# Performance work log

Measured on AMD Instinct MI355X. Metric: run time of the kernel, lower is better.

The kernel has to match this reference:

```python
import jax, jax.numpy as jnp
import numpy as np

UNITS = 512
GROUPS = 32
EPS = 1e-5


def group_norm(x, w, b, groups=GROUPS, eps=EPS):
    B, C, H, W = x.shape
    xg = x.reshape(B, groups, C // groups, H, W)
    mean = xg.mean(axis=(2, 3, 4), keepdims=True)
    var = ((xg - mean) ** 2).mean(axis=(2, 3, 4), keepdims=True)
    xg = (xg - mean) * jax.lax.rsqrt(var + eps)
    return xg.reshape(B, C, H, W) * w[None, :, None, None] + b[None, :, None, None]


def conv1x1(x, w, b):
    # w: [out_ch, in_ch], b: [out_ch]
    return jnp.einsum('oc,bchw->bohw', w, x) + b[None, :, None, None]


def setup_inputs() -> dict:
    key = jax.random.key(0)
    ks = jax.random.split(key, 11)
    C = UNITS
    s = 1.0 / np.sqrt(C)
    return {
        'x': jax.random.normal(ks[0], (16, C, 64, 64), dtype=jnp.float32),
        'gn_w': jnp.ones((C,), dtype=jnp.float32),
        'gn_b': jnp.zeros((C,), dtype=jnp.float32),
        'wq': jax.random.normal(ks[1], (C, C), dtype=jnp.float32) * s,
        'bq': jnp.zeros((C,), dtype=jnp.float32),
        'wk': jax.random.normal(ks[2], (C, C), dtype=jnp.float32) * s,
        'bk': jnp.zeros((C,), dtype=jnp.float32),
        'wv': jax.random.normal(ks[3], (C, C), dtype=jnp.float32) * s,
        'bv': jnp.zeros((C,), dtype=jnp.float32),
        'wp': jax.random.normal(ks[4], (C, C), dtype=jnp.float32) * s,
        'bp': jnp.zeros((C,), dtype=jnp.float32),
    }


def reference(x, gn_w, gn_b, wq, bq, wk, bk, wv, bv, wp, bp):
    B, C, H, W = x.shape
    g = GROUPS
    xn = group_norm(x, gn_w, gn_b)
    q = conv1x1(xn, wq, bq).reshape(B, g, C // g, H * W)
    k = conv1x1(xn, wk, bk).reshape(B, g, C // g, H * W)
    v = conv1x1(xn, wv, bv).reshape(B, g, C // g, H * W)
    # channel attention: scores over per-group channel dims, spatial contracted
    attn = jnp.einsum('bgci,bgdi->bgcd', q, k) / jnp.sqrt(jnp.float32(C))
    attn = jax.nn.softmax(attn, axis=-1)
    out = jnp.einsum('bgcd,bgdi->bgci', attn, v).reshape(B, C, H, W)
    # NB: original adds proj(out) to out (not a residual to the input)
    return out + conv1x1(out, wp, bp)
```

## Files before the change

### kernel.cpp

```cpp
#include <hip/hip_runtime.h>

typedef __attribute__((ext_vector_type(8))) short bf16x8;
typedef __attribute__((ext_vector_type(4))) float f32x4;
typedef __attribute__((ext_vector_type(8))) unsigned short us8;
typedef unsigned short u16;
typedef unsigned int u32;

__device__ __forceinline__ u16 f2bf(float f){
  u32 u = __builtin_bit_cast(u32, f);
  u32 r = (u + 0x7fffu + ((u >> 16) & 1u)) >> 16;
  return (u16)r;
}

#define ASYNC_CP16(gp, lp) __builtin_amdgcn_global_load_lds( \
    (__attribute__((address_space(1))) void*)(gp), \
    (__attribute__((address_space(3))) void*)(lp), 16, 0, 0)

__device__ const int d_rt[10] = {0,0,0,0,1,1,1,2,2,3};
__device__ const int d_ct[10] = {0,1,2,3,1,2,3,2,3,3};

__global__ __launch_bounds__(256) void k_stats(const float* __restrict__ x,
    const float* __restrict__ gnw, const float* __restrict__ gnb,
    u16* __restrict__ xb, float* __restrict__ a, float* __restrict__ cv,
    float* __restrict__ sx)
{
  int b = blockIdx.x >> 5;
  int g = blockIdx.x & 31;
  int tid = threadIdx.x;
  int cl = tid >> 4;
  int l16 = tid & 15;
  int c = g * 16 + cl;
  const float* xp = x + ((long)(b * 512 + c)) * 4096;
  u16* xbp = xb + ((long)(b * 512 + c)) * 4096;
  float s = 0.f, sq = 0.f;
  for (int it = 0; it < 64; ++it) {
    int i4 = it * 16 + l16;
    float4 v = *(const float4*)(xp + i4 * 4);
    s  += v.x + v.y + v.z + v.w;
    sq += v.x * v.x + v.y * v.y + v.z * v.z + v.w * v.w;
    ushort4 o;
    o.x = f2bf(v.x); o.y = f2bf(v.y); o.z = f2bf(v.z); o.w = f2bf(v.w);
    *(ushort4*)(xbp + i4 * 4) = o;
  }
  for (int off = 8; off; off >>= 1) { s += __shfl_xor(s, off); sq += __shfl_xor(sq, off); }
  __shared__ float chS[16], chQ[16];
  if (l16 == 0) { chS[cl] = s; chQ[cl] = sq; }
  __syncthreads();
  if (tid < 16) {
    float S = 0.f, Q = 0.f;
    for (int j = 0; j < 16; ++j) { S += chS[j]; Q += chQ[j]; }
    float mean = S * (1.f / 65536.f);
    float var  = Q * (1.f / 65536.f) - mean * mean;
    float rs = rsqrtf(var + 1e-5f);
    int cc = g * 16 + tid;
    float av = gnw[cc] * rs;
    a[b * 512 + cc]  = av;
    cv[b * 512 + cc] = gnb[cc] - mean * av;
    sx[b * 512 + cc] = chS[tid];
  }
}

__global__ __launch_bounds__(256) void k_wconv(const float* __restrict__ wq,
    const float* __restrict__ wp, u16* __restrict__ wqb, u16* __restrict__ wpb)
{
  int i = blockIdx.x * 256 + threadIdx.x;
  wqb[i] = f2bf(wq[i]);
  wpb[i] = f2bf(wp[i]);
}

__global__ __launch_bounds__(256) void k_transpose(const u16* __restrict__ xb,
                                                   u16* __restrict__ xT)
{
  __shared__ u16 t[64][72];
  int i0 = blockIdx.x * 64, e0 = blockIdx.y * 64, b = blockIdx.z;
  int tid = threadIdx.x;
  #pragma unroll
  for (int p = 0; p < 2; ++p) {
    int task = p * 256 + tid;
    int er = task >> 3, ic = (task & 7) * 8;
    us8 v = *(const us8*)(xb + ((long)(b * 512 + e0 + er)) * 4096 + i0 + ic);
    #pragma unroll
    for (int j = 0; j < 8; ++j) t[ic + j][er] = v[j];
  }
  __syncthreads();
  #pragma unroll
  for (int p = 0; p < 2; ++p) {
    int task = p * 256 + tid;
    int ir = task >> 3, ec = (task & 7) * 8;
    us8 w = *(const us8*)&t[ir][ec];
    *(us8*)(xT + ((long)(b * 4096 + i0 + ir)) * 512 + e0 + ec) = w;
  }
}

__global__ __launch_bounds__(256) void k_gram_split(const u16* __restrict__ xb,
                                                    float* __restrict__ part)
{
  __shared__ u16 As[128 * 64];
  __shared__ u16 Bs[128 * 64];
  const int tid = threadIdx.x;
  const int wave = tid >> 6, lane = tid & 63;
  const int tile = blockIdx.x % 10, split = blockIdx.x / 10;
  const int b = blockIdx.y;
  const int tm = d_rt[tile] * 128, tn = d_ct[tile] * 128;
  const u16* Xb = xb + (long)b * 512 * 4096;
  const int wm = (wave >> 1) << 6, wn = (wave & 1) << 6;
  const int l15 = lane & 15, l4 = lane >> 4;

  f32x4 acc[4][4];
  f32x4 z = {0.f, 0.f, 0.f, 0.f};
  #pragma unroll
  for (int fm = 0; fm < 4; ++fm)
    #pragma unroll
    for (int fn = 0; fn < 4; ++fn) acc[fm][fn] = z;

  const int qa = wave * 4;
  const int srow = lane >> 3;
  const int scol = (lane & 7) * 8;
  const int k0 = split * 1024;

  for (int kt = k0; kt < k0 + 1024; kt += 64) {
    #pragma unroll
    for (int j = 0; j < 4; ++j) {
      int q = qa + j;
      const u16* gpA = Xb + (long)(tm + q * 8 + srow) * 4096 + kt + scol;
      ASYNC_CP16(gpA, &As[q * 512]);
      const u16* gpB = Xb + (long)(tn + q * 8 + srow) * 4096 + kt + scol;
      ASYNC_CP16(gpB, &Bs[q * 512]);
    }
    __syncthreads();
    #pragma unroll
    for (int kk = 0; kk < 64; kk += 32) {
      bf16x8 af[4], bfr[4];
      #pragma unroll
      for (int f = 0; f < 4; ++f) {
        af[f]  = *(const bf16x8*)&As[(wm + f * 16 + l15) * 64 + kk + l4 * 8];
        bfr[f] = *(const bf16x8*)&Bs[(wn + f * 16 + l15) * 64 + kk + l4 * 8];
      }
      #pragma unroll
      for (int fm = 0; fm < 4; ++fm)
        #pragma unroll
        for (int fn = 0; fn < 4; ++fn)
          acc[fm][fn] = __builtin_amdgcn_mfma_f32_16x16x32_bf16(
              af[fm], bfr[fn], acc[fm][fn], 0, 0, 0);
    }
    __syncthreads();
  }

  float* pp = part + ((((long)split * 16 + b) * 10 + tile) << 14);
  #pragma unroll
  for (int fm = 0; fm < 4; ++fm)
    #pragma unroll
    for (int fn = 0; fn < 4; ++fn)
      #pragma unroll
      for (int r = 0; r < 4; ++r)
        pp[(wm + fm * 16 + l4 * 4 + r) * 128 + wn + fn * 16 + l15] =
            acc[fm][fn][r];
}

__global__ __launch_bounds__(512) void k_gram_reduce(
    const float* __restrict__ part, const float* __restrict__ a,
    u16* __restrict__ Gp)
{
  const int tile = blockIdx.x, b = blockIdx.y;
  const int tmt = d_rt[tile], tnt = d_ct[tile];
  const int tm = tmt * 128, tn = tnt * 128;
  const int tid = threadIdx.x;
  __shared__ u16 t[128][130];
  const float* p0 = part + (((long)b * 10 + tile) << 14);
  const long ss = (long)16 * 10 * 16384;
  u16* Gb = Gp + (long)b * 262144;
  const float acol = a[b * 512 + tn + (tid & 127)];
  for (int chunk = 0; chunk < 32; ++chunk) {
    int idx = chunk * 512 + tid;
    int row = idx >> 7, col = idx & 127;
    float v = p0[idx] + p0[idx + ss] + p0[idx + 2 * ss] + p0[idx + 3 * ss];
    v *= a[b * 512 + tm + row] * acol;
    u16 bf = f2bf(v);
    Gb[(tm + row) * 512 + tn + col] = bf;
    t[row][col] = bf;
  }
  if (tmt != tnt) {
    __syncthreads();
    for (int chunk = 0; chunk < 32; ++chunk) {
      int idx = chunk * 512 + tid;
      int row = idx >> 7, col = idx & 127;
      Gb[(tn + row) * 512 + tm + col] = t[col][row];
    }
  }
}

template<int EPI>
__global__ __launch_bounds__(256) void k_ntgemm(
    const u16* __restrict__ A, long sA, int lda,
    const u16* __restrict__ B, long sB, int ldb,
    int K, int ntn,
    float* __restrict__ fout, long sF, int ldf,
    u16* __restrict__ bout, long sO, int ldo_,
    const float* __restrict__ ascale,
    const float* __restrict__ cinit,
    const float* __restrict__ cadd)
{
  __shared__ u16 As[128 * 64];
  __shared__ u16 Bs[128 * 64];
  const int tid = threadIdx.x;
  const int wave = tid >> 6, lane = tid & 63;
  const int b = blockIdx.y;
  const int tm = (blockIdx.x / ntn) * 128, tn = (blockIdx.x % ntn) * 128;
  const u16* Ab = A + sA * b;
  const u16* Bb = B + sB * b;
  const int wm = (wave >> 1) << 6, wn = (wave & 1) << 6;
  const int l15 = lane & 15, l4 = lane >> 4;

  f32x4 acc[4][4];
  if (EPI == 2) {
    const float* Cb = cinit + (long)b * 262144;
    #pragma unroll
    for (int fm = 0; fm < 4; ++fm)
      #pragma unroll
      for (int fn = 0; fn < 4; ++fn)
        #pragma unroll
        for (int r = 0; r < 4; ++r) {
          int row = tm + wm + fm * 16 + l4 * 4 + r;
          int col = tn + wn + fn * 16 + l15;
          acc[fm][fn][r] = Cb[row * 512 + col];
        }
  } else {
    f32x4 z = {0.f, 0.f, 0.f, 0.f};
    #pragma unroll
    for (int fm = 0; fm < 4; ++fm)
      #pragma unroll
      for (int fn = 0; fn < 4; ++fn) acc[fm][fn] = z;
  }

  const int qa = wave * 4;
  const int srow = lane >> 3;
  const int scol = (lane & 7) * 8;

  for (int kt = 0; kt < K; kt += 64) {
    #pragma unroll
    for (int j = 0; j < 4; ++j) {
      int q = qa + j;
      const u16* gpA = Ab + (long)(tm + q * 8 + srow) * lda + kt + scol;
      ASYNC_CP16(gpA, &As[q * 512]);
      const u16* gpB = Bb + (long)(tn + q * 8 + srow) * ldb + kt + scol;
      ASYNC_CP16(gpB, &Bs[q * 512]);
    }
    __syncthreads();
    #pragma unroll
    for (int kk = 0; kk < 64; kk += 32) {
      bf16x8 af[4], bfr[4];
      #pragma unroll
      for (int f = 0; f < 4; ++f) {
        af[f]  = *(const bf16x8*)&As[(wm + f * 16 + l15) * 64 + kk + l4 * 8];
        bfr[f] = *(const bf16x8*)&Bs[(wn + f * 16 + l15) * 64 + kk + l4 * 8];
      }
      #pragma unroll
      for (int fm = 0; fm < 4; ++fm)
        #pragma unroll
        for (int fn = 0; fn < 4; ++fn)
          acc[fm][fn] = __builtin_amdgcn_mfma_f32_16x16x32_bf16(
              af[fm], bfr[fn], acc[fm][fn], 0, 0, 0);
    }
    __syncthreads();
  }

  #pragma unroll
  for (int fm = 0; fm < 4; ++fm)
    #pragma unroll
    for (int fn = 0; fn < 4; ++fn)
      #pragma unroll
      for (int r = 0; r < 4; ++r) {
        int row = tm + wm + fm * 16 + l4 * 4 + r;
        int col = tn + wn + fn * 16 + l15;
        float v = acc[fm][fn][r];
        if (EPI == 1) {
          fout[sF * b + (long)row * ldf + col] = v;
        } else if (EPI == 2) {
          v *= ascale[b * 512 + col];
          bout[sO * b + (long)row * ldo_ + col] = f2bf(v);
        } else {
          fout[sF * b + (long)row * ldf + col] = v + cadd[b * 512 + row];
        }
      }
}

__global__ __launch_bounds__(256) void k_vec(
    const float* __restrict__ wq, const float* __restrict__ bq,
    const float* __restrict__ wk, const float* __restrict__ bk,
    const float* __restrict__ wv, const float* __restrict__ bv,
    const float* __restrict__ a, const float* __restrict__ cv,
    const float* __restrict__ sx,
    float* __restrict__ eq, float* __restrict__ uq, float* __restrict__ ek,
    float* __restrict__ uk, float* __restrict__ hv)
{
  int b = blockIdx.x / 5, which = blockIdx.x % 5;
  __shared__ float vec[512];
  int tid = threadIdx.x;
  for (int i = tid; i < 512; i += 256)
    vec[i] = (which == 1 || which == 3) ? a[b * 512 + i] * sx[b * 512 + i]
                                        : cv[b * 512 + i];
  __syncthreads();
  const float* W = (which < 2) ? wq : (which < 4) ? wk : wv;
  const float* bias = (which == 0) ? bq : (which == 2) ? bk : (which == 4) ? bv : nullptr;
  float* outp = (which == 0) ? eq : (which == 1) ? uq : (which == 2) ? ek
              : (which == 3) ? uk : hv;
  for (int c = tid; c < 512; c += 256) {
    const float* wr = W + (long)c * 512;
    float s2 = 0.f;
    for (int e = 0; e < 512; e += 4) {
      float4 w4 = *(const float4*)(wr + e);
      s2 += w4.x * vec[e] + w4.y * vec[e + 1] + w4.z * vec[e + 2] + w4.w * vec[e + 3];
    }
    if (bias) s2 += bias[c];
    outp[b * 512 + c] = s2;
  }
}

__global__ __launch_bounds__(256) void k_scores(
    const float* __restrict__ P,
    const float* __restrict__ wk, const float* __restrict__ wv,
    const float* __restrict__ eq, const float* __restrict__ uq,
    const float* __restrict__ ek, const float* __restrict__ uk,
    const float* __restrict__ hv,
    float* __restrict__ U, u16* __restrict__ UT, float* __restrict__ oc)
{
  int b = blockIdx.x >> 5, g = blockIdx.x & 31;
  int tid = threadIdx.x;
  __shared__ float Pl[16 * 516];
  __shared__ float Wl[16 * 516];
  __shared__ float at[16][16];

  const float* Pb = P + (long)b * 262144 + g * 16 * 512;
  for (int t = tid; t < 16 * 128; t += 256) {
    int r = t >> 7, q = t & 127;
    *(float4*)&Pl[r * 516 + q * 4] = *(const float4*)(Pb + r * 512 + q * 4);
  }
  const float* Wkb = wk + (long)g * 16 * 512;
  for (int t = tid; t < 16 * 128; t += 256) {
    int r = t >> 7, q = t & 127;
    *(float4*)&Wl[r * 516 + q * 4] = *(const float4*)(Wkb + r * 512 + q * 4);
  }
  __syncthreads();

  int c = tid >> 4, d = tid & 15;
  float s0 = 0.f;
  for (int e = 0; e < 512; e += 4) {
    float4 p4 = *(const float4*)&Pl[c * 516 + e];
    float4 w4 = *(const float4*)&Wl[d * 516 + e];
    s0 += p4.x * w4.x + p4.y * w4.y + p4.z * w4.z + p4.w * w4.w;
  }
  float eqc = eq[b * 512 + g * 16 + c], uqc = uq[b * 512 + g * 16 + c];
  float ekd = ek[b * 512 + g * 16 + d], ukd = uk[b * 512 + g * 16 + d];
  float s = (s0 + eqc * ukd + uqc * ekd + 4096.f * eqc * ekd) * 0.04419417382415922f;
  float m = s;
  for (int off = 8; off; off >>= 1) m = fmaxf(m, __shfl_xor(m, off));
  float p = expf(s - m);
  float sum = p;
  for (int off = 8; off; off >>= 1) sum += __shfl_xor(sum, off);
  at[c][d] = p / sum;
  __syncthreads();

  const float* Wvb = wv + (long)g * 16 * 512;
  for (int t = tid; t < 16 * 128; t += 256) {
    int r = t >> 7, q = t & 127;
    *(float4*)&Wl[r * 516 + q * 4] = *(const float4*)(Wvb + r * 512 + q * 4);
  }
  __syncthreads();

  float* Ub = U + (long)b * 262144 + g * 16 * 512;
  for (int t = 0; t < 32; ++t) {
    int flat = t * 256 + tid;
    int cc = flat >> 9, e = flat & 511;
    float a2 = 0.f;
    #pragma unroll
    for (int dd = 0; dd < 16; ++dd) a2 += at[cc][dd] * Wl[dd * 516 + e];
    Ub[cc * 512 + e] = a2;
    Pl[cc * 516 + e] = a2;
  }
  if (tid < 16) {
    float o2 = 0.f;
    #pragma unroll
    for (int dd = 0; dd < 16; ++dd) o2 += at[tid][dd] * hv[b * 512 + g * 16 + dd];
    oc[b * 512 + g * 16 + tid] = o2;
  }
  __syncthreads();
  for (int t = 0; t < 32; ++t) {
    int flat = t * 256 + tid;
    int cc = flat & 15, e = flat >> 4;
    UT[(long)b * 262144 + e * 512 + g * 16 + cc] = f2bf(Pl[cc * 516 + e]);
  }
}

__global__ __launch_bounds__(256) void k_c3(const float* __restrict__ wp,
    const float* __restrict__ bp, const float* __restrict__ oc,
    float* __restrict__ c3)
{
  int b = blockIdx.x >> 1;
  int o = (blockIdx.x & 1) * 256 + threadIdx.x;
  __shared__ float ov[512];
  for (int i = threadIdx.x; i < 512; i += 256) ov[i] = oc[b * 512 + i];
  __syncthreads();
  const float* wr = wp + (long)o * 512;
  float s = 0.f;
  for (int e = 0; e < 512; e += 4) {
    float4 w4 = *(const float4*)(wr + e);
    s += w4.x * ov[e] + w4.y * ov[e + 1] + w4.z * ov[e + 2] + w4.w * ov[e + 3];
  }
  c3[b * 512 + o] = oc[b * 512 + o] + s + bp[o];
}

extern "C" void kernel_launch(void* const* d_in, const int* in_sizes, int n_in,
                              void* d_out, int out_size, void* d_ws, size_t ws_size,
                              hipStream_t stream)
{
  (void)in_sizes; (void)n_in; (void)out_size; (void)ws_size;
  const float* x   = (const float*)d_in[0];
  const float* gnw = (const float*)d_in[1];
  const float* gnb = (const float*)d_in[2];
  const float* wq  = (const float*)d_in[3];
  const float* bq  = (const float*)d_in[4];
  const float* wk  = (const float*)d_in[5];
  const float* bk  = (const float*)d_in[6];
  const float* wv  = (const float*)d_in[7];
  const float* bv  = (const float*)d_in[8];
  const float* wp  = (const float*)d_in[9];
  const float* bp  = (const float*)d_in[10];
  float* out = (float*)d_out;

  char* ws = (char*)d_ws;
  u16* xT  = (u16*)ws;  ws += (size_t)16 * 4096 * 512 * 2;
  u16* Gp  = (u16*)ws;  ws += (size_t)16 * 512 * 512 * 2;
  float* P = (float*)ws; ws += (size_t)16 * 512 * 512 * 4;
  float* U = (float*)ws; ws += (size_t)16 * 512 * 512 * 4;
  u16* UT  = (u16*)ws;  ws += (size_t)16 * 512 * 512 * 2;
  u16* W3  = (u16*)ws;  ws += (size_t)16 * 512 * 512 * 2;
  u16* wqb = (u16*)ws;  ws += (size_t)512 * 512 * 2;
  u16* wpb = (u16*)ws;  ws += (size_t)512 * 512 * 2;
  float* a  = (float*)ws; ws += 16 * 512 * 4;
  float* cv = (float*)ws; ws += 16 * 512 * 4;
  float* sx = (float*)ws; ws += 16 * 512 * 4;
  float* eq = (float*)ws; ws += 16 * 512 * 4;
  float* uq = (float*)ws; ws += 16 * 512 * 4;
  float* ek = (float*)ws; ws += 16 * 512 * 4;
  float* uk = (float*)ws; ws += 16 * 512 * 4;
  float* hv = (float*)ws; ws += 16 * 512 * 4;
  float* oc = (float*)ws; ws += 16 * 512 * 4;
  float* c3 = (float*)ws; ws += 16 * 512 * 4;

  u16* xb = (u16*)d_out;
  float* part = (float*)xT;

  k_stats<<<512, 256, 0, stream>>>(x, gnw, gnb, xb, a, cv, sx);
  k_wconv<<<1024, 256, 0, stream>>>(wq, wp, wqb, wpb);
  k_gram_split<<<dim3(40, 16), 256, 0, stream>>>(xb, part);
  k_gram_reduce<<<dim3(10, 16), 512, 0, stream>>>(part, a, Gp);
  k_transpose<<<dim3(64, 8, 16), 256, 0, stream>>>(xb, xT);
  k_vec<<<80, 256, 0, stream>>>(wq, bq, wk, bk, wv, bv, a, cv, sx,
                                eq, uq, ek, uk, hv);
  k_ntgemm<1><<<dim3(16, 16), 256, 0, stream>>>(
      wqb, 0, 512, Gp, 262144, 512, 512, 4,
      P, 262144, 512, nullptr, 0, 0, nullptr, nullptr, nullptr);
  k_scores<<<512, 256, 0, stream>>>(P, wk, wv, eq, uq, ek, uk, hv, U, UT, oc);
  k_c3<<<32, 256, 0, stream>>>(wp, bp, oc, c3);
  k_ntgemm<2><<<dim3(16, 16), 256, 0, stream>>>(
      wpb, 0, 512, UT, 262144, 512, 512, 4,
      nullptr, 0, 0, W3, 262144, 512, a, U, nullptr);
  k_ntgemm<3><<<dim3(128, 16), 256, 0, stream>>>(
      W3, 262144, 512, xT, (long)4096 * 512, 512, 512, 32,
      out, (long)512 * 4096, 4096, nullptr, 0, 0, nullptr, nullptr, c3);
}
```

Baseline: 299.6 us.

## Double-buffer LDS in GEMM kernels, share diagonal gram tiles, store P as bf16

Both the gram-split and generic NT GEMM kernels now use two LDS buffers, so the next K-tile's async global-to-LDS copy is issued while the current tile feeds the MFMAs. Diagonal gram tiles load only the A tile and reuse it as B, which halves their global traffic. The intermediate P matrix is written as bf16 instead of fp32 and widened back to fp32 in k_scores, cutting its memory traffic at some cost in precision. Doubling LDS use (64KB per block) may lower occupancy. The loop issues the next stage's async writes without waiting on them before reading the current buffer, which depends on the implicit vmcnt handling of global_load_lds.

```diff
diff --git a/kernel.cpp b/kernel.cpp
--- a/kernel.cpp
+++ b/kernel.cpp
@@ -10,6 +10,9 @@
   u32 u = __builtin_bit_cast(u32, f);
   u32 r = (u + 0x7fffu + ((u >> 16) & 1u)) >> 16;
   return (u16)r;
+}
+__device__ __forceinline__ float bf2f(u16 h){
+  return __builtin_bit_cast(float, (u32)h << 16);
 }
 
 #define ASYNC_CP16(gp, lp) __builtin_amdgcn_global_load_lds( \
@@ -95,12 +98,13 @@
 __global__ __launch_bounds__(256) void k_gram_split(const u16* __restrict__ xb,
                                                     float* __restrict__ part)
 {
-  __shared__ u16 As[128 * 64];
-  __shared__ u16 Bs[128 * 64];
+  __shared__ u16 As[2][128 * 64];
+  __shared__ u16 Bs[2][128 * 64];
   const int tid = threadIdx.x;
   const int wave = tid >> 6, lane = tid & 63;
   const int tile = blockIdx.x % 10, split = blockIdx.x / 10;
   const int b = blockIdx.y;
+  const bool diag = (d_rt[tile] == d_ct[tile]);
   const int tm = d_rt[tile] * 128, tn = d_ct[tile] * 128;
   const u16* Xb = xb + (long)b * 512 * 4096;
   const int wm = (wave >> 1) << 6, wn = (wave & 1) << 6;
@@ -116,25 +120,34 @@
   const int qa = wave * 4;
   const int srow = lane >> 3;
   const int scol = (lane & 7) * 8;
-  const int k0 = split * 1024;
-
-  for (int kt = k0; kt < k0 + 1024; kt += 64) {
+  const int k0 = split * 1024, kend = k0 + 1024;
+
+  auto STAGE = [&](int buf, int kt) {
     #pragma unroll
     for (int j = 0; j < 4; ++j) {
       int q = qa + j;
-      const u16* gpA = Xb + (long)(tm + q * 8 + srow) * 4096 + kt + scol;
-      ASYNC_CP16(gpA, &As[q * 512]);
-      const u16* gpB = Xb + (long)(tn + q * 8 + srow) * 4096 + kt + scol;
-      ASYNC_CP16(gpB, &Bs[q * 512]);
-    }
-    __syncthreads();
+      ASYNC_CP16(Xb + (long)(tm + q * 8 + srow) * 4096 + kt + scol,
+                 &As[buf][q * 512]);
+      if (!diag)
+        ASYNC_CP16(Xb + (long)(tn + q * 8 + srow) * 4096 + kt + scol,
+                   &Bs[buf][q * 512]);
+    }
+  };
+
+  STAGE(0, k0);
+  __syncthreads();
+  int cur = 0;
+  for (int kt = k0; kt < kend; kt += 64) {
+    if (kt + 64 < kend) STAGE(cur ^ 1, kt + 64);
+    const u16* cA = &As[cur][0];
+    const u16* cB = diag ? cA : &Bs[cur][0];
     #pragma unroll
     for (int kk = 0; kk < 64; kk += 32) {
       bf16x8 af[4], bfr[4];
       #pragma unroll
       for (int f = 0; f < 4; ++f) {
-        af[f]  = *(const bf16x8*)&As[(wm + f * 16 + l15) * 64 + kk + l4 * 8];
-        bfr[f] = *(const bf16x8*)&Bs[(wn + f * 16 + l15) * 64 + kk + l4 * 8];
+        af[f]  = *(const bf16x8*)&cA[(wm + f * 16 + l15) * 64 + kk + l4 * 8];
+        bfr[f] = *(const bf16x8*)&cB[(wn + f * 16 + l15) * 64 + kk + l4 * 8];
       }
       #pragma unroll
       for (int fm = 0; fm < 4; ++fm)
@@ -144,6 +157,7 @@
               af[fm], bfr[fn], acc[fm][fn], 0, 0, 0);
     }
     __syncthreads();
+    cur ^= 1;
   }
 
   float* pp = part + ((((long)split * 16 + b) * 10 + tile) << 14);
@@ -200,8 +214,8 @@
     const float* __restrict__ cinit,
     const float* __restrict__ cadd)
 {
-  __shared__ u16 As[128 * 64];
-  __shared__ u16 Bs[128 * 64];
+  __shared__ u16 As[2][128 * 64];
+  __shared__ u16 Bs[2][128 * 64];
   const int tid = threadIdx.x;
   const int wave = tid >> 6, lane = tid & 63;
   const int b = blockIdx.y;
@@ -236,23 +250,29 @@
   const int srow = lane >> 3;
   const int scol = (lane & 7) * 8;
 
-  for (int kt = 0; kt < K; kt += 64) {
+  auto STAGE = [&](int buf, int kt) {
     #pragma unroll
     for (int j = 0; j < 4; ++j) {
       int q = qa + j;
-      const u16* gpA = Ab + (long)(tm + q * 8 + srow) * lda + kt + scol;
-      ASYNC_CP16(gpA, &As[q * 512]);
-      const u16* gpB = Bb + (long)(tn + q * 8 + srow) * ldb + kt + scol;
-      ASYNC_CP16(gpB, &Bs[q * 512]);
-    }
-    __syncthreads();
+      ASYNC_CP16(Ab + (long)(tm + q * 8 + srow) * lda + kt + scol,
+                 &As[buf][q * 512]);
+      ASYNC_CP16(Bb + (long)(tn + q * 8 + srow) * ldb + kt + scol,
+                 &Bs[buf][q * 512]);
+    }
+  };
+
+  STAGE(0, 0);
+  __syncthreads();
+  int cur = 0;
+  for (int kt = 0; kt < K; kt += 64) {
+    if (kt + 64 < K) STAGE(cur ^ 1, kt + 64);
     #pragma unroll
     for (int kk = 0; kk < 64; kk += 32) {
       bf16x8 af[4], bfr[4];
       #pragma unroll
       for (int f = 0; f < 4; ++f) {
-        af[f]  = *(const bf16x8*)&As[(wm + f * 16 + l15) * 64 + kk + l4 * 8];
-        bfr[f] = *(const bf16x8*)&Bs[(wn + f * 16 + l15) * 64 + kk + l4 * 8];
+        af[f]  = *(const bf16x8*)&As[cur][(wm + f * 16 + l15) * 64 + kk + l4 * 8];
+        bfr[f] = *(const bf16x8*)&Bs[cur][(wn + f * 16 + l15) * 64 + kk + l4 * 8];
       }
       #pragma unroll
       for (int fm = 0; fm < 4; ++fm)
@@ -262,6 +282,7 @@
               af[fm], bfr[fn], acc[fm][fn], 0, 0, 0);
     }
     __syncthreads();
+    cur ^= 1;
   }
 
   #pragma unroll
@@ -274,7 +295,7 @@
         int col = tn + wn + fn * 16 + l15;
         float v = acc[fm][fn][r];
         if (EPI == 1) {
-          fout[sF * b + (long)row * ldf + col] = v;
+          bout[sO * b + (long)row * ldo_ + col] = f2bf(v);
         } else if (EPI == 2) {
           v *= ascale[b * 512 + col];
           bout[sO * b + (long)row * ldo_ + col] = f2bf(v);
@@ -317,7 +338,7 @@
 }
 
 __global__ __launch_bounds__(256) void k_scores(
-    const float* __restrict__ P,
+    const u16* __restrict__ P,
     const float* __restrict__ wk, const float* __restrict__ wv,
     const float* __restrict__ eq, const float* __restrict__ uq,
     const float* __restrict__ ek, const float* __restrict__ uk,
@@ -330,10 +351,12 @@
   __shared__ float Wl[16 * 516];
   __shared__ float at[16][16];
 
-  const float* Pb = P + (long)b * 262144 + g * 16 * 512;
-  for (int t = tid; t < 16 * 128; t += 256) {
-    int r = t >> 7, q = t & 127;
-    *(float4*)&Pl[r * 516 + q * 4] = *(const float4*)(Pb + r * 512 + q * 4);
+  const u16* Pb = P + (long)b * 262144 + g * 16 * 512;
+  for (int t = tid; t < 1024; t += 256) {
+    int r = t >> 6, q = (t & 63) * 8;
+    us8 v = *(const us8*)(Pb + r * 512 + q);
+    #pragma unroll
+    for (int j = 0; j < 8; ++j) Pl[r * 516 + q + j] = bf2f(v[j]);
   }
   const float* Wkb = wk + (long)g * 16 * 512;
   for (int t = tid; t < 16 * 128; t += 256) {
@@ -430,7 +453,7 @@
   char* ws = (char*)d_ws;
   u16* xT  = (u16*)ws;  ws += (size_t)16 * 4096 * 512 * 2;
   u16* Gp  = (u16*)ws;  ws += (size_t)16 * 512 * 512 * 2;
-  float* P = (float*)ws; ws += (size_t)16 * 512 * 512 * 4;
+  u16* P   = (u16*)ws;  ws += (size_t)16 * 512 * 512 * 2;
   float* U = (float*)ws; ws += (size_t)16 * 512 * 512 * 4;
   u16* UT  = (u16*)ws;  ws += (size_t)16 * 512 * 512 * 2;
   u16* W3  = (u16*)ws;  ws += (size_t)16 * 512 * 512 * 2;
@@ -459,7 +482,7 @@
                                 eq, uq, ek, uk, hv);
   k_ntgemm<1><<<dim3(16, 16), 256, 0, stream>>>(
       wqb, 0, 512, Gp, 262144, 512, 512, 4,
-      P, 262144, 512, nullptr, 0, 0, nullptr, nullptr, nullptr);
+      nullptr, 0, 0, P, 262144, 512, nullptr, nullptr, nullptr);
   k_scores<<<512, 256, 0, stream>>>(P, wk, wv, eq, uq, ek, uk, hv, U, UT, oc);
   k_c3<<<32, 256, 0, stream>>>(wp, bp, oc, c3);
   k_ntgemm<2><<<dim3(16, 16), 256, 0, stream>>>(
```

Result: no change. 300.3 us (+0.2%).
